# Performance work log

Measured on AMD Instinct MI355X. Metric: run time of the kernel, lower is better.

The kernel has to match this reference:

```python
import jax, jax.numpy as jnp
import numpy as np

HEADS = 8

def setup_inputs() -> dict:
    key = jax.random.key(0)
    ks = jax.random.split(key, 10)
    B, C, D, W, H = 4, 256, 12, 12, 12
    dk = C // HEADS
    return {
        "x": jax.random.normal(ks[0], (B, C, D, W, H), jnp.float32),
        "wq": jax.random.normal(ks[1], (C, C), jnp.float32) * 0.05,
        "bq": jax.random.normal(ks[2], (C,), jnp.float32) * 0.05,
        "wk": jax.random.normal(ks[3], (C, C), jnp.float32) * 0.05,
        "bk": jax.random.normal(ks[4], (C,), jnp.float32) * 0.05,
        "wv": jax.random.normal(ks[5], (C, C), jnp.float32) * 0.05,
        "bv": jax.random.normal(ks[6], (C,), jnp.float32) * 0.05,
        "rel_d": jax.random.normal(ks[7], (1, HEADS, dk, D, 1, 1), jnp.float32),
        "rel_h": jax.random.normal(ks[8], (1, HEADS, dk, 1, 1, H), jnp.float32),
        "rel_w": jax.random.normal(ks[9], (1, HEADS, dk, 1, W, 1), jnp.float32),
    }


def reference(x, wq, bq, wk, bk, wv, bv, rel_d, rel_h, rel_w):
    B, C, D, W, H = x.shape
    dk = C // HEADS
    N = D * W * H

    def proj(w, b):
        # Conv3d kernel_size=1 == per-voxel linear over channels
        y = jnp.einsum('bcdwh,oc->bodwh', x, w) + b[None, :, None, None, None]
        return y.reshape(B, HEADS, dk, N)  # [B,h,dk,N]

    q = proj(wq, bq)
    k = proj(wk, bk)
    v = proj(wv, bv)

    # content-content: q^T k -> [B,h,N,N]
    cc = jnp.einsum('bhdn,bhdm->bhnm', q, k)
    # relative-position bias: (rel_h+rel_w+rel_d) broadcasts to [1,h,dk,D,W,H]
    pos = (rel_h + rel_w + rel_d).reshape(1, HEADS, dk, N)
    # content-position: pos^T @ q -> [B,h,N,N]
    cp = jnp.einsum('bhdn,bhdm->bhnm', pos, q)

    attn = jax.nn.softmax(cc + cp, axis=-1)  # [B,h,N,N]
    # out = v @ attn^T -> [B,h,dk,N]
    out = jnp.einsum('bhdn,bhmn->bhdm', v, attn)
    return out.reshape(B, C, D, W, H)
```

## Files before the change

### kernel.cpp

```cpp
#include <hip/hip_runtime.h>
#include <math.h>

#define HEADS 8
#define DK 32
#define B_ 4
#define C_ 256
#define NVOX 1728
#define DE 64
#define PITCH 72
#define XPITCH 136
#define CPITCH 36
#define LOG2E 1.44269504088896f

typedef _Float16 f16x8 __attribute__((ext_vector_type(8)));
typedef __fp16 fp16x2 __attribute__((ext_vector_type(2)));
typedef float f32x16 __attribute__((ext_vector_type(16)));

__device__ inline float h2f(short s) {
    _Float16 h = *(_Float16*)&s;
    return (float)h;
}
__device__ inline f32x16 mfma32h(f16x8 a, f16x8 b, f32x16 c) {
    return __builtin_amdgcn_mfma_f32_32x32x16_f16(a, b, c, 0, 0, 0);
}

union H8 { _Float16 h[8]; uint4 v; };

__global__ __launch_bounds__(256)
void prep_kernel(const float* __restrict__ x,
                 const float* __restrict__ wq, const float* __restrict__ wk,
                 const float* __restrict__ wv,
                 const float* __restrict__ rel_d, const float* __restrict__ rel_h,
                 const float* __restrict__ rel_w,
                 short* __restrict__ wf, short* __restrict__ xf,
                 short* __restrict__ Qf) {
    __shared__ float tile[64][65];
    int bid = blockIdx.x;
    int t = threadIdx.x;

    if (bid < 768) {
        int idx = bid * 256 + t;
        int m = idx >> 16;
        const float* w = (m == 0) ? wq : (m == 1) ? wk : wv;
        _Float16 h = (_Float16)w[idx & 65535];
        wf[idx] = *(short*)&h;
    } else if (bid < 1200) {
        int q = bid - 768;
        int nb = (q % 27) * 64;
        int c0 = ((q / 27) % 4) * 64;
        int b  = q / 108;
        const float* xb = x + (size_t)b * C_ * NVOX;
        for (int e = t; e < 4096; e += 256) {
            int ci = e >> 6, nl = e & 63;
            tile[ci][nl] = xb[(size_t)(c0 + ci) * NVOX + nb + nl];
        }
        __syncthreads();
        for (int e = t; e < 512; e += 256) {
            int n = e >> 3, cg = (e & 7) * 8;
            H8 hi;
            #pragma unroll
            for (int j = 0; j < 8; j++) hi.h[j] = (_Float16)tile[cg + j][n];
            *(uint4*)&xf[((size_t)b * NVOX + nb + n) * C_ + c0 + cg] = hi.v;
        }
    } else {
        int q = bid - 1200;
        int nb = (q % 27) * 64;
        int h  = (q / 27) % 8;
        int b  = q / 216;
        int bh = b * HEADS + h;
        int nl = t & 63, dd0 = (t >> 6) * 8;
        int n = nb + nl;
        int di = n / 144, wi = (n / 12) % 12, hi = n % 12;
        H8 ph;
        #pragma unroll
        for (int o = 0; o < 8; o++) {
            int hd = h * DK + dd0 + o;
            ph.h[o] = (_Float16)(rel_d[hd * 12 + di] + rel_w[hd * 12 + wi] +
                                 rel_h[hd * 12 + hi]);
        }
        *(uint4*)&Qf[((size_t)bh * NVOX + n) * DE + DK + dd0] = ph.v;
    }
}

struct FS {
    union {
        short xs[64 * XPITCH];
        float cbuf[3][64][CPITCH];
    } u;
};

__global__ __launch_bounds__(384, 4)
void fproj_kernel(const short* __restrict__ xf, const short* __restrict__ wf,
                  const float* __restrict__ bq, const float* __restrict__ bk,
                  const float* __restrict__ bv,
                  short* __restrict__ Qf, short* __restrict__ Kf,
                  short* __restrict__ Vf) {
    __shared__ FS sm;
    int nb = blockIdx.x * 64, h = blockIdx.y, b = blockIdx.z;
    int bh = b * HEADS + h;
    int t = threadIdx.x;
    int w = t >> 6, l = t & 63, ln = l & 31, hv = l >> 5;
    int mat = w >> 1, nh = w & 1;

    const short* xb = xf + ((size_t)b * NVOX + nb) * C_;
    const short* wA = wf + ((size_t)mat * C_ + h * DK + ln) * C_;
    int xrow = (nh * 32 + ln) * XPITCH;

    f32x16 acc;
    #pragma unroll
    for (int r = 0; r < 16; r++) acc[r] = 0.f;

    #pragma unroll 1
    for (int ch = 0; ch < 2; ch++) {
        __syncthreads();
        for (int e = t; e < 1024; e += 384) {
            int row = e >> 4, c8 = (e & 15) * 8;
            *(uint4*)&sm.u.xs[row * XPITCH + c8] =
                *(const uint4*)&xb[row * C_ + ch * 128 + c8];
        }
        __syncthreads();
        #pragma unroll 4
        for (int ks = 0; ks < 8; ks++) {
            int kl_ = ks * 16 + hv * 8;
            f16x8 a = *(const f16x8*)&wA[ch * 128 + kl_];
            f16x8 bfr = *(const f16x8*)&sm.u.xs[xrow + kl_];
            acc = mfma32h(a, bfr, acc);
        }
    }
    __syncthreads();

    const float* bias = (mat == 0) ? bq : (mat == 1) ? bk : bv;
    int ncol = nh * 32 + ln;
    #pragma unroll
    for (int q2 = 0; q2 < 4; q2++) {
        float4 cv;
        float* cvp = (float*)&cv;
        #pragma unroll
        for (int m = 0; m < 4; m++) {
            int o_loc = 8 * q2 + 4 * hv + m;
            cvp[m] = acc[4 * q2 + m] + bias[h * DK + o_loc];
        }
        *(float4*)&sm.u.cbuf[mat][ncol][8 * q2 + 4 * hv] = cv;
    }
    __syncthreads();

    if (t < 256) {
        int n = t >> 2, ddg = (t & 3) * 8;
        size_t rowoff = ((size_t)bh * NVOX + nb + n) * DE;
        H8 qh, kh;
        #pragma unroll
        for (int j = 0; j < 8; j++) {
            qh.h[j] = (_Float16)sm.u.cbuf[0][n][ddg + j];
            kh.h[j] = (_Float16)sm.u.cbuf[1][n][ddg + j];
        }
        *(uint4*)&Qf[rowoff + ddg] = qh.v;
        *(uint4*)&Kf[rowoff + ddg] = kh.v;
        *(uint4*)&Kf[rowoff + DK + ddg] = qh.v;
    }
    if (t < 256) {
        int d = t >> 3, ng = (t & 7) * 8;
        H8 vv;
        #pragma unroll
        for (int j = 0; j < 8; j++)
            vv.h[j] = (_Float16)sm.u.cbuf[2][ng + j][d];
        *(uint4*)&Vf[((size_t)bh * DK + d) * NVOX + nb + ng] = vv.v;
    }
}

struct SMem {
    short K[64][PITCH];
    short V[DK][PITCH];
    short P[64][PITCH];
};

__global__ __launch_bounds__(128, 3)
void attn_kernel(const short* __restrict__ Qf, const short* __restrict__ Kf,
                 const short* __restrict__ Vf,
                 short* __restrict__ wsO, float* __restrict__ wsM,
                 float* __restrict__ wsL) {
    __shared__ SMem sm;
    int bx = blockIdx.x;
    int it = bx >> 1, jp = bx & 1;
    int h = blockIdx.y, b = blockIdx.z;
    int bh = b * HEADS + h;
    int t = threadIdx.x;
    int w  = t >> 6;
    int l  = t & 63;
    int ln = l & 31;
    int hv = l >> 5;
    int i_loc  = w * 32 + ln;
    int i_glob = it * 64 + i_loc;

    const short* Qp = Qf + (size_t)bh * NVOX * DE;
    const short* Kp = Kf + (size_t)bh * NVOX * DE;
    const short* Vp = Vf + (size_t)bh * DK * NVOX;

    f16x8 qf[4];
    #pragma unroll
    for (int ks = 0; ks < 4; ks++)
        qf[ks] = *(const f16x8*)&Qp[(size_t)i_glob * DE + ks * 16 + hv * 8];

    float mL = -INFINITY;
    float lsum = 0.f;
    f32x16 O;
    #pragma unroll
    for (int r = 0; r < 16; r++) O[r] = 0.f;

    int jt0 = jp ? 14 : 0, jt1 = jp ? 27 : 14;
    #pragma unroll 1
    for (int jt = jt0; jt < jt1; jt++) {
        int jb = jt * 64;
        __syncthreads();
        for (int e = t; e < 512; e += 128) {
            int row = e >> 3, c = (e & 7) * 8;
            *(uint4*)&sm.K[row][c] = *(const uint4*)&Kp[(size_t)(jb + row) * DE + c];
        }
        for (int e = t; e < 256; e += 128) {
            int d = e >> 3, c = (e & 7) * 8;
            *(uint4*)&sm.V[d][c] = *(const uint4*)&Vp[(size_t)d * NVOX + jb + c];
        }
        __syncthreads();

        f32x16 sc[2];
        #pragma unroll
        for (int js = 0; js < 2; js++) {
            f32x16 s;
            #pragma unroll
            for (int r = 0; r < 16; r++) s[r] = 0.f;
            #pragma unroll
            for (int ks = 0; ks < 4; ks++) {
                f16x8 kfr = *(const f16x8*)&sm.K[js * 32 + ln][ks * 16 + hv * 8];
                s = mfma32h(kfr, qf[ks], s);
            }
            sc[js] = s;
        }

        float mx = sc[0][0];
        #pragma unroll
        for (int js = 0; js < 2; js++)
            #pragma unroll
            for (int r = 0; r < 16; r++) mx = fmaxf(mx, sc[js][r]);
        mx = fmaxf(mx, __shfl_xor(mx, 32));
        float mLn = fmaxf(mL, mx * LOG2E);
        float alpha = exp2f(mL - mLn);
        mL = mLn;
        float ps = 0.f;
        #pragma unroll
        for (int js = 0; js < 2; js++)
            #pragma unroll
            for (int r = 0; r < 16; r++) {
                float p = exp2f(fmaf(sc[js][r], LOG2E, -mLn));
                sc[js][r] = p;
                ps += p;
            }
        ps += __shfl_xor(ps, 32);
        lsum = lsum * alpha + ps;

        #pragma unroll
        for (int js = 0; js < 2; js++)
            #pragma unroll
            for (int g = 0; g < 4; g++) {
                union { fp16x2 h2[2]; uint2 v; } pk;
                pk.h2[0] = __builtin_amdgcn_cvt_pkrtz(sc[js][4 * g + 0], sc[js][4 * g + 1]);
                pk.h2[1] = __builtin_amdgcn_cvt_pkrtz(sc[js][4 * g + 2], sc[js][4 * g + 3]);
                *(uint2*)&sm.P[i_loc][js * 32 + g * 8 + hv * 4] = pk.v;
            }

        #pragma unroll
        for (int r = 0; r < 16; r++) O[r] *= alpha;
        #pragma unroll
        for (int ks = 0; ks < 4; ks++) {
            f16x8 va = *(const f16x8*)&sm.V[ln][ks * 16 + hv * 8];
            f16x8 pb = *(const f16x8*)&sm.P[i_loc][ks * 16 + hv * 8];
            O = mfma32h(va, pb, O);
        }
    }

    short* Op = wsO + ((size_t)jp * (B_ * HEADS) + bh) * DK * NVOX;
    #pragma unroll
    for (int r = 0; r < 16; r++) {
        int d = (r & 3) + 8 * (r >> 2) + 4 * hv;
        _Float16 oh = (_Float16)O[r];
        Op[(size_t)d * NVOX + i_glob] = *(short*)&oh;
    }
    if (hv == 0) {
        size_t mo = ((size_t)jp * (B_ * HEADS) + bh) * NVOX + i_glob;
        wsM[mo] = mL;
        wsL[mo] = lsum;
    }
}

__global__ void combine_kernel(const short* __restrict__ wsO,
                               const float* __restrict__ wsM,
                               const float* __restrict__ wsL,
                               float* __restrict__ out) {
    int idx = blockIdx.x * 256 + threadIdx.x;
    int i = idx % NVOX;
    int bh = (idx / NVOX) >> 5;
    const size_t oh = (size_t)B_ * HEADS * DK * NVOX;
    const size_t mh = (size_t)B_ * HEADS * NVOX;
    size_t mo = (size_t)bh * NVOX + i;
    float m0 = wsM[mo], m1 = wsM[mh + mo];
    float l0 = wsL[mo], l1 = wsL[mh + mo];
    float m = fmaxf(m0, m1);
    float a0 = exp2f(m0 - m), a1 = exp2f(m1 - m);
    float num = a0 * h2f(wsO[idx]) + a1 * h2f(wsO[oh + idx]);
    float den = a0 * l0 + a1 * l1;
    out[idx] = num / den;
}

extern "C" void kernel_launch(void* const* d_in, const int* in_sizes, int n_in,
                              void* d_out, int out_size, void* d_ws, size_t ws_size,
                              hipStream_t stream) {
    const float* x     = (const float*)d_in[0];
    const float* wq    = (const float*)d_in[1];
    const float* bq    = (const float*)d_in[2];
    const float* wk    = (const float*)d_in[3];
    const float* bk    = (const float*)d_in[4];
    const float* wv    = (const float*)d_in[5];
    const float* bv    = (const float*)d_in[6];
    const float* rel_d = (const float*)d_in[7];
    const float* rel_h = (const float*)d_in[8];
    const float* rel_w = (const float*)d_in[9];
    float* out = (float*)d_out;

    size_t qksz = (size_t)B_ * HEADS * NVOX * DE;
    size_t vsz  = (size_t)B_ * HEADS * DK * NVOX;
    short* Qf  = (short*)d_ws;
    short* Kf  = Qf + qksz;
    short* Vf  = Kf + qksz;
    short* wf  = Vf + vsz;
    short* wsO = wf + (size_t)3 * C_ * C_;
    float* wsM = (float*)(wsO + 2 * vsz);
    float* wsL = wsM + 2 * (size_t)B_ * HEADS * NVOX;
    short* xf  = wsO;

    prep_kernel<<<dim3(2064), dim3(256), 0, stream>>>(
        x, wq, wk, wv, rel_d, rel_h, rel_w, wf, xf, Qf);
    fproj_kernel<<<dim3(NVOX / 64, HEADS, B_), dim3(384), 0, stream>>>(
        xf, wf, bq, bk, bv, Qf, Kf, Vf);
    attn_kernel<<<dim3(2 * NVOX / 64, HEADS, B_), dim3(128), 0, stream>>>(
        Qf, Kf, Vf, wsO, wsM, wsL);
    combine_kernel<<<dim3((int)(vsz / 256)), dim3(256), 0, stream>>>(wsO, wsM, wsL, out);
}
```

Baseline: 159.0 us.

## Fuse prep into projection and split-K combine into attention via atomic counter

Removes the separate prep kernel: the projection kernel now reads fp32 x and weights directly, converts them to fp16 on the fly (transposing x through shared memory), and also writes the positional half of Q. The combine kernel is also removed: the second attention block to finish each tile, detected with an atomic counter plus threadfences, merges both partial softmax results and writes the final output. This cuts two launches and the intermediate xf/wf round trips through memory. In exchange, each projection block redundantly converts weights and x, shared-memory stores in the transpose are scalar and may bank-conflict, occupancy hint drops from 4 to 3, and a memset launch is added.

```diff
diff --git a/kernel.cpp b/kernel.cpp
--- a/kernel.cpp
+++ b/kernel.cpp
@@ -24,63 +24,7 @@
     return __builtin_amdgcn_mfma_f32_32x32x16_f16(a, b, c, 0, 0, 0);
 }
 
-union H8 { _Float16 h[8]; uint4 v; };
-
-__global__ __launch_bounds__(256)
-void prep_kernel(const float* __restrict__ x,
-                 const float* __restrict__ wq, const float* __restrict__ wk,
-                 const float* __restrict__ wv,
-                 const float* __restrict__ rel_d, const float* __restrict__ rel_h,
-                 const float* __restrict__ rel_w,
-                 short* __restrict__ wf, short* __restrict__ xf,
-                 short* __restrict__ Qf) {
-    __shared__ float tile[64][65];
-    int bid = blockIdx.x;
-    int t = threadIdx.x;
-
-    if (bid < 768) {
-        int idx = bid * 256 + t;
-        int m = idx >> 16;
-        const float* w = (m == 0) ? wq : (m == 1) ? wk : wv;
-        _Float16 h = (_Float16)w[idx & 65535];
-        wf[idx] = *(short*)&h;
-    } else if (bid < 1200) {
-        int q = bid - 768;
-        int nb = (q % 27) * 64;
-        int c0 = ((q / 27) % 4) * 64;
-        int b  = q / 108;
-        const float* xb = x + (size_t)b * C_ * NVOX;
-        for (int e = t; e < 4096; e += 256) {
-            int ci = e >> 6, nl = e & 63;
-            tile[ci][nl] = xb[(size_t)(c0 + ci) * NVOX + nb + nl];
-        }
-        __syncthreads();
-        for (int e = t; e < 512; e += 256) {
-            int n = e >> 3, cg = (e & 7) * 8;
-            H8 hi;
-            #pragma unroll
-            for (int j = 0; j < 8; j++) hi.h[j] = (_Float16)tile[cg + j][n];
-            *(uint4*)&xf[((size_t)b * NVOX + nb + n) * C_ + c0 + cg] = hi.v;
-        }
-    } else {
-        int q = bid - 1200;
-        int nb = (q % 27) * 64;
-        int h  = (q / 27) % 8;
-        int b  = q / 216;
-        int bh = b * HEADS + h;
-        int nl = t & 63, dd0 = (t >> 6) * 8;
-        int n = nb + nl;
-        int di = n / 144, wi = (n / 12) % 12, hi = n % 12;
-        H8 ph;
-        #pragma unroll
-        for (int o = 0; o < 8; o++) {
-            int hd = h * DK + dd0 + o;
-            ph.h[o] = (_Float16)(rel_d[hd * 12 + di] + rel_w[hd * 12 + wi] +
-                                 rel_h[hd * 12 + hi]);
-        }
-        *(uint4*)&Qf[((size_t)bh * NVOX + n) * DE + DK + dd0] = ph.v;
-    }
-}
+union HF8 { _Float16 h[8]; f16x8 f; uint4 v; };
 
 struct FS {
     union {
@@ -89,10 +33,14 @@
     } u;
 };
 
-__global__ __launch_bounds__(384, 4)
-void fproj_kernel(const short* __restrict__ xf, const short* __restrict__ wf,
+__global__ __launch_bounds__(384, 3)
+void fproj_kernel(const float* __restrict__ x,
+                  const float* __restrict__ wq, const float* __restrict__ wk,
+                  const float* __restrict__ wv,
                   const float* __restrict__ bq, const float* __restrict__ bk,
                   const float* __restrict__ bv,
+                  const float* __restrict__ rel_d, const float* __restrict__ rel_h,
+                  const float* __restrict__ rel_w,
                   short* __restrict__ Qf, short* __restrict__ Kf,
                   short* __restrict__ Vf) {
     __shared__ FS sm;
@@ -102,8 +50,9 @@
     int w = t >> 6, l = t & 63, ln = l & 31, hv = l >> 5;
     int mat = w >> 1, nh = w & 1;
 
-    const short* xb = xf + ((size_t)b * NVOX + nb) * C_;
-    const short* wA = wf + ((size_t)mat * C_ + h * DK + ln) * C_;
+    const float* xb = x + (size_t)b * C_ * NVOX + nb;
+    const float* wsel = (mat == 0) ? wq : (mat == 1) ? wk : wv;
+    const float* wrow = wsel + (size_t)(h * DK + ln) * C_;
     int xrow = (nh * 32 + ln) * XPITCH;
 
     f32x16 acc;
@@ -112,19 +61,38 @@
 
     #pragma unroll 1
     for (int ch = 0; ch < 2; ch++) {
+        f16x8 wfr[8];
+        #pragma unroll
+        for (int ks = 0; ks < 8; ks++) {
+            const float* wp = wrow + ch * 128 + ks * 16 + hv * 8;
+            float4 a4 = *(const float4*)&wp[0];
+            float4 b4 = *(const float4*)&wp[4];
+            HF8 hh;
+            hh.h[0] = (_Float16)a4.x; hh.h[1] = (_Float16)a4.y;
+            hh.h[2] = (_Float16)a4.z; hh.h[3] = (_Float16)a4.w;
+            hh.h[4] = (_Float16)b4.x; hh.h[5] = (_Float16)b4.y;
+            hh.h[6] = (_Float16)b4.z; hh.h[7] = (_Float16)b4.w;
+            wfr[ks] = hh.f;
+        }
+
         __syncthreads();
-        for (int e = t; e < 1024; e += 384) {
-            int row = e >> 4, c8 = (e & 15) * 8;
-            *(uint4*)&sm.u.xs[row * XPITCH + c8] =
-                *(const uint4*)&xb[row * C_ + ch * 128 + c8];
+        for (int e = t; e < 2048; e += 384) {
+            int cl = e >> 4;
+            int n4 = (e & 15) * 4;
+            float4 v = *(const float4*)&xb[(size_t)(ch * 128 + cl) * NVOX + n4];
+            _Float16 h0 = (_Float16)v.x, h1 = (_Float16)v.y,
+                     h2 = (_Float16)v.z, h3 = (_Float16)v.w;
+            sm.u.xs[(n4 + 0) * XPITCH + cl] = *(short*)&h0;
+            sm.u.xs[(n4 + 1) * XPITCH + cl] = *(short*)&h1;
+            sm.u.xs[(n4 + 2) * XPITCH + cl] = *(short*)&h2;
+            sm.u.xs[(n4 + 3) * XPITCH + cl] = *(short*)&h3;
         }
         __syncthreads();
-        #pragma unroll 4
+
+        #pragma unroll
         for (int ks = 0; ks < 8; ks++) {
-            int kl_ = ks * 16 + hv * 8;
-            f16x8 a = *(const f16x8*)&wA[ch * 128 + kl_];
-            f16x8 bfr = *(const f16x8*)&sm.u.xs[xrow + kl_];
-            acc = mfma32h(a, bfr, acc);
+            f16x8 bfr = *(const f16x8*)&sm.u.xs[xrow + ks * 16 + hv * 8];
+            acc = mfma32h(wfr[ks], bfr, acc);
         }
     }
     __syncthreads();
@@ -145,25 +113,40 @@
     __syncthreads();
 
     if (t < 256) {
-        int n = t >> 2, ddg = (t & 3) * 8;
-        size_t rowoff = ((size_t)bh * NVOX + nb + n) * DE;
-        H8 qh, kh;
-        #pragma unroll
-        for (int j = 0; j < 8; j++) {
-            qh.h[j] = (_Float16)sm.u.cbuf[0][n][ddg + j];
-            kh.h[j] = (_Float16)sm.u.cbuf[1][n][ddg + j];
-        }
-        *(uint4*)&Qf[rowoff + ddg] = qh.v;
-        *(uint4*)&Kf[rowoff + ddg] = kh.v;
-        *(uint4*)&Kf[rowoff + DK + ddg] = qh.v;
-    }
-    if (t < 256) {
-        int d = t >> 3, ng = (t & 7) * 8;
-        H8 vv;
-        #pragma unroll
-        for (int j = 0; j < 8; j++)
-            vv.h[j] = (_Float16)sm.u.cbuf[2][ng + j][d];
-        *(uint4*)&Vf[((size_t)bh * DK + d) * NVOX + nb + ng] = vv.v;
+        {
+            int n = t >> 2, ddg = (t & 3) * 8;
+            size_t rowoff = ((size_t)bh * NVOX + nb + n) * DE;
+            HF8 qh, kh;
+            #pragma unroll
+            for (int j = 0; j < 8; j++) {
+                qh.h[j] = (_Float16)sm.u.cbuf[0][n][ddg + j];
+                kh.h[j] = (_Float16)sm.u.cbuf[1][n][ddg + j];
+            }
+            *(uint4*)&Qf[rowoff + ddg] = qh.v;
+            *(uint4*)&Kf[rowoff + ddg] = kh.v;
+            *(uint4*)&Kf[rowoff + DK + ddg] = qh.v;
+        }
+        {
+            int d = t >> 3, ng = (t & 7) * 8;
+            HF8 vv;
+            #pragma unroll
+            for (int j = 0; j < 8; j++)
+                vv.h[j] = (_Float16)sm.u.cbuf[2][ng + j][d];
+            *(uint4*)&Vf[((size_t)bh * DK + d) * NVOX + nb + ng] = vv.v;
+        }
+        {
+            int nl = t & 63, dd0 = (t >> 6) * 8;
+            int n = nb + nl;
+            int di = n / 144, wi = (n / 12) % 12, hi = n % 12;
+            HF8 ph;
+            #pragma unroll
+            for (int o = 0; o < 8; o++) {
+                int hd = h * DK + dd0 + o;
+                ph.h[o] = (_Float16)(rel_d[hd * 12 + di] + rel_w[hd * 12 + wi] +
+                                     rel_h[hd * 12 + hi]);
+            }
+            *(uint4*)&Qf[((size_t)bh * NVOX + n) * DE + DK + dd0] = ph.v;
+        }
     }
 }
 
@@ -177,8 +160,10 @@
 void attn_kernel(const short* __restrict__ Qf, const short* __restrict__ Kf,
                  const short* __restrict__ Vf,
                  short* __restrict__ wsO, float* __restrict__ wsM,
-                 float* __restrict__ wsL) {
+                 float* __restrict__ wsL, int* __restrict__ cnt,
+                 float* __restrict__ out) {
     __shared__ SMem sm;
+    __shared__ int lastFlag;
     int bx = blockIdx.x;
     int it = bx >> 1, jp = bx & 1;
     int h = blockIdx.y, b = blockIdx.z;
@@ -276,6 +261,12 @@
         }
     }
 
+    #pragma unroll
+    for (int r = 0; r < 16; r++) {
+        _Float16 t16 = (_Float16)O[r];
+        O[r] = (float)t16;
+    }
+
     short* Op = wsO + ((size_t)jp * (B_ * HEADS) + bh) * DK * NVOX;
     #pragma unroll
     for (int r = 0; r < 16; r++) {
@@ -288,25 +279,29 @@
         wsM[mo] = mL;
         wsL[mo] = lsum;
     }
-}
-
-__global__ void combine_kernel(const short* __restrict__ wsO,
-                               const float* __restrict__ wsM,
-                               const float* __restrict__ wsL,
-                               float* __restrict__ out) {
-    int idx = blockIdx.x * 256 + threadIdx.x;
-    int i = idx % NVOX;
-    int bh = (idx / NVOX) >> 5;
-    const size_t oh = (size_t)B_ * HEADS * DK * NVOX;
-    const size_t mh = (size_t)B_ * HEADS * NVOX;
-    size_t mo = (size_t)bh * NVOX + i;
-    float m0 = wsM[mo], m1 = wsM[mh + mo];
-    float l0 = wsL[mo], l1 = wsL[mh + mo];
-    float m = fmaxf(m0, m1);
-    float a0 = exp2f(m0 - m), a1 = exp2f(m1 - m);
-    float num = a0 * h2f(wsO[idx]) + a1 * h2f(wsO[oh + idx]);
-    float den = a0 * l0 + a1 * l1;
-    out[idx] = num / den;
+
+    __threadfence();
+    __syncthreads();
+    if (t == 0) lastFlag = atomicAdd(&cnt[bh * 27 + it], 1);
+    __syncthreads();
+    if (lastFlag == 0) return;
+    __threadfence();
+
+    int jpo = jp ^ 1;
+    size_t moo = ((size_t)jpo * (B_ * HEADS) + bh) * NVOX + i_glob;
+    float mo_ = wsM[moo];
+    float lo_ = wsL[moo];
+    float m = fmaxf(mL, mo_);
+    float a_s = exp2f(mL - m), a_o = exp2f(mo_ - m);
+    float inv = 1.f / (a_s * lsum + a_o * lo_);
+    const short* Po = wsO + ((size_t)jpo * (B_ * HEADS) + bh) * DK * NVOX;
+    float* outp = out + (size_t)bh * DK * NVOX;
+    #pragma unroll
+    for (int r = 0; r < 16; r++) {
+        int d = (r & 3) + 8 * (r >> 2) + 4 * hv;
+        float oo = h2f(Po[(size_t)d * NVOX + i_glob]);
+        outp[(size_t)d * NVOX + i_glob] = (a_s * O[r] + a_o * oo) * inv;
+    }
 }
 
 extern "C" void kernel_launch(void* const* d_in, const int* in_sizes, int n_in,
@@ -326,20 +321,18 @@
 
     size_t qksz = (size_t)B_ * HEADS * NVOX * DE;
     size_t vsz  = (size_t)B_ * HEADS * DK * NVOX;
+    size_t mlsz = (size_t)B_ * HEADS * NVOX;
     short* Qf  = (short*)d_ws;
     short* Kf  = Qf + qksz;
     short* Vf  = Kf + qksz;
-    short* wf  = Vf + vsz;
-    short* wsO = wf + (size_t)3 * C_ * C_;
+    short* wsO = Vf + vsz;
     float* wsM = (float*)(wsO + 2 * vsz);
-    float* wsL = wsM + 2 * (size_t)B_ * HEADS * NVOX;
-    short* xf  = wsO;
-
-    prep_kernel<<<dim3(2064), dim3(256), 0, stream>>>(
-        x, wq, wk, wv, rel_d, rel_h, rel_w, wf, xf, Qf);
+    float* wsL = wsM + 2 * mlsz;
+    int*   cnt = (int*)(wsL + 2 * mlsz);
+
+    hipMemsetAsync(cnt, 0, (size_t)B_ * HEADS * 27 * sizeof(int), stream);
     fproj_kernel<<<dim3(NVOX / 64, HEADS, B_), dim3(384), 0, stream>>>(
-        xf, wf, bq, bk, bv, Qf, Kf, Vf);
+        x, wq, wk, wv, bq, bk, bv, rel_d, rel_h, rel_w, Qf, Kf, Vf);
     attn_kernel<<<dim3(2 * NVOX / 64, HEADS, B_), dim3(128), 0, stream>>>(
-        Qf, Kf, Vf, wsO, wsM, wsL);
-    combine_kernel<<<dim3((int)(vsz / 256)), dim3(256), 0, stream>>>(wsO, wsM, wsL, out);
-}
+        Qf, Kf, Vf, wsO, wsM, wsL, cnt, out);
+}
```

After: 367.9 us. +131.3%, slower.

## Prefetch next K/V tile into registers in attention loop; vectorize prep and combine

Applied to the files above, without the earlier changes.

The attention kernel now loads the next K/V tile from global memory into registers at the start of each iteration and writes it to shared memory after the compute. This hides global load latency behind the MFMA work instead of stalling at the start of every tile. Separately, the weight-conversion part of prep and the combine kernel now process four elements per thread with vector loads and stores, which cuts the grid sizes. The prefetch uses extra registers and adds a second barrier per iteration.

```diff
diff --git a/kernel.cpp b/kernel.cpp
--- a/kernel.cpp
+++ b/kernel.cpp
@@ -25,6 +25,7 @@
 }
 
 union H8 { _Float16 h[8]; uint4 v; };
+union H4 { _Float16 h[4]; uint2 v; };
 
 __global__ __launch_bounds__(256)
 void prep_kernel(const float* __restrict__ x,
@@ -38,14 +39,17 @@
     int bid = blockIdx.x;
     int t = threadIdx.x;
 
-    if (bid < 768) {
-        int idx = bid * 256 + t;
+    if (bid < 192) {
+        int idx = (bid * 256 + t) * 4;
         int m = idx >> 16;
         const float* w = (m == 0) ? wq : (m == 1) ? wk : wv;
-        _Float16 h = (_Float16)w[idx & 65535];
-        wf[idx] = *(short*)&h;
-    } else if (bid < 1200) {
-        int q = bid - 768;
+        float4 v = *(const float4*)&w[idx & 65535];
+        H4 hh;
+        hh.h[0] = (_Float16)v.x; hh.h[1] = (_Float16)v.y;
+        hh.h[2] = (_Float16)v.z; hh.h[3] = (_Float16)v.w;
+        *(uint2*)&wf[idx] = hh.v;
+    } else if (bid < 624) {
+        int q = bid - 192;
         int nb = (q % 27) * 64;
         int c0 = ((q / 27) % 4) * 64;
         int b  = q / 108;
@@ -63,7 +67,7 @@
             *(uint4*)&xf[((size_t)b * NVOX + nb + n) * C_ + c0 + cg] = hi.v;
         }
     } else {
-        int q = bid - 1200;
+        int q = bid - 624;
         int nb = (q % 27) * 64;
         int h  = (q / 27) % 8;
         int b  = q / 216;
@@ -206,20 +210,41 @@
     #pragma unroll
     for (int r = 0; r < 16; r++) O[r] = 0.f;
 
+    int krow0 = t >> 3, kcol = (t & 7) * 8;
+    int vrow0 = t >> 3;
+    uint4 kr[4], vr[2];
+
     int jt0 = jp ? 14 : 0, jt1 = jp ? 27 : 14;
+
+    {
+        int jb = jt0 * 64;
+        #pragma unroll
+        for (int q = 0; q < 4; q++)
+            kr[q] = *(const uint4*)&Kp[(size_t)(jb + krow0 + q * 16) * DE + kcol];
+        #pragma unroll
+        for (int q = 0; q < 2; q++)
+            vr[q] = *(const uint4*)&Vp[(size_t)(vrow0 + q * 16) * NVOX + jb + kcol];
+        #pragma unroll
+        for (int q = 0; q < 4; q++)
+            *(uint4*)&sm.K[krow0 + q * 16][kcol] = kr[q];
+        #pragma unroll
+        for (int q = 0; q < 2; q++)
+            *(uint4*)&sm.V[vrow0 + q * 16][kcol] = vr[q];
+    }
+
     #pragma unroll 1
     for (int jt = jt0; jt < jt1; jt++) {
-        int jb = jt * 64;
-        __syncthreads();
-        for (int e = t; e < 512; e += 128) {
-            int row = e >> 3, c = (e & 7) * 8;
-            *(uint4*)&sm.K[row][c] = *(const uint4*)&Kp[(size_t)(jb + row) * DE + c];
-        }
-        for (int e = t; e < 256; e += 128) {
-            int d = e >> 3, c = (e & 7) * 8;
-            *(uint4*)&sm.V[d][c] = *(const uint4*)&Vp[(size_t)d * NVOX + jb + c];
-        }
-        __syncthreads();
+        __syncthreads();
+        bool more = (jt + 1 < jt1);
+        if (more) {
+            int jb = (jt + 1) * 64;
+            #pragma unroll
+            for (int q = 0; q < 4; q++)
+                kr[q] = *(const uint4*)&Kp[(size_t)(jb + krow0 + q * 16) * DE + kcol];
+            #pragma unroll
+            for (int q = 0; q < 2; q++)
+                vr[q] = *(const uint4*)&Vp[(size_t)(vrow0 + q * 16) * NVOX + jb + kcol];
+        }
 
         f32x16 sc[2];
         #pragma unroll
@@ -274,6 +299,16 @@
             f16x8 pb = *(const f16x8*)&sm.P[i_loc][ks * 16 + hv * 8];
             O = mfma32h(va, pb, O);
         }
+
+        __syncthreads();
+        if (more) {
+            #pragma unroll
+            for (int q = 0; q < 4; q++)
+                *(uint4*)&sm.K[krow0 + q * 16][kcol] = kr[q];
+            #pragma unroll
+            for (int q = 0; q < 2; q++)
+                *(uint4*)&sm.V[vrow0 + q * 16][kcol] = vr[q];
+        }
     }
 
     short* Op = wsO + ((size_t)jp * (B_ * HEADS) + bh) * DK * NVOX;
@@ -294,19 +329,32 @@
                                const float* __restrict__ wsM,
                                const float* __restrict__ wsL,
                                float* __restrict__ out) {
-    int idx = blockIdx.x * 256 + threadIdx.x;
+    int idx = (blockIdx.x * 256 + threadIdx.x) * 4;
     int i = idx % NVOX;
     int bh = (idx / NVOX) >> 5;
     const size_t oh = (size_t)B_ * HEADS * DK * NVOX;
     const size_t mh = (size_t)B_ * HEADS * NVOX;
     size_t mo = (size_t)bh * NVOX + i;
-    float m0 = wsM[mo], m1 = wsM[mh + mo];
-    float l0 = wsL[mo], l1 = wsL[mh + mo];
-    float m = fmaxf(m0, m1);
-    float a0 = exp2f(m0 - m), a1 = exp2f(m1 - m);
-    float num = a0 * h2f(wsO[idx]) + a1 * h2f(wsO[oh + idx]);
-    float den = a0 * l0 + a1 * l1;
-    out[idx] = num / den;
+    float4 m0 = *(const float4*)&wsM[mo];
+    float4 m1 = *(const float4*)&wsM[mh + mo];
+    float4 l0 = *(const float4*)&wsL[mo];
+    float4 l1 = *(const float4*)&wsL[mh + mo];
+    uint2 o0u = *(const uint2*)&wsO[idx];
+    uint2 o1u = *(const uint2*)&wsO[oh + idx];
+    const short* o0s = (const short*)&o0u;
+    const short* o1s = (const short*)&o1u;
+    const float* m0p = (const float*)&m0; const float* m1p = (const float*)&m1;
+    const float* l0p = (const float*)&l0; const float* l1p = (const float*)&l1;
+    float4 res;
+    float* rp = (float*)&res;
+    #pragma unroll
+    for (int j = 0; j < 4; j++) {
+        float m = fmaxf(m0p[j], m1p[j]);
+        float a0 = exp2f(m0p[j] - m), a1 = exp2f(m1p[j] - m);
+        rp[j] = (a0 * h2f(o0s[j]) + a1 * h2f(o1s[j])) /
+                (a0 * l0p[j] + a1 * l1p[j]);
+    }
+    *(float4*)&out[idx] = res;
 }
 
 extern "C" void kernel_launch(void* const* d_in, const int* in_sizes, int n_in,
@@ -335,11 +383,11 @@
     float* wsL = wsM + 2 * (size_t)B_ * HEADS * NVOX;
     short* xf  = wsO;
 
-    prep_kernel<<<dim3(2064), dim3(256), 0, stream>>>(
+    prep_kernel<<<dim3(1488), dim3(256), 0, stream>>>(
         x, wq, wk, wv, rel_d, rel_h, rel_w, wf, xf, Qf);
     fproj_kernel<<<dim3(NVOX / 64, HEADS, B_), dim3(384), 0, stream>>>(
         xf, wf, bq, bk, bv, Qf, Kf, Vf);
     attn_kernel<<<dim3(2 * NVOX / 64, HEADS, B_), dim3(128), 0, stream>>>(
         Qf, Kf, Vf, wsO, wsM, wsL);
-    combine_kernel<<<dim3((int)(vsz / 256)), dim3(256), 0, stream>>>(wsO, wsM, wsL, out);
-}
+    combine_kernel<<<dim3((int)(vsz / 1024)), dim3(256), 0, stream>>>(wsO, wsM, wsL, out);
+}
```

Result: slower. 187.6 us (+18.0%).
